# Kernel tuning notes

Hardware: AMD Instinct MI355X
Metric: run time of the kernel (lower is better)

The kernel has to match this reference:

```python
import jax, jax.numpy as jnp
import numpy as np
import math

E = 8          # num_exp
K = 2          # top-k
IN_D = 1024
HD = 2048
BS = 8
SEQ = 2048
CAP_FACTOR = 1.25
MIN_CAP = 4


def setup_inputs() -> dict:
    key = jax.random.key(0)
    ks = jax.random.split(key, 5)
    s = 0.02  # init scale for weights
    x = jax.random.normal(ks[0], (BS, SEQ, IN_D), jnp.float32)
    gate_w = jax.random.normal(ks[1], (E, IN_D), jnp.float32) * s
    fc1_w = jax.random.normal(ks[2], (E, HD, IN_D), jnp.float32) * s
    gating_w = jax.random.normal(ks[3], (E, HD, IN_D), jnp.float32) * s
    fc2_w = jax.random.normal(ks[4], (E, IN_D, HD), jnp.float32) * s
    return {"x": x, "gate_w": gate_w, "fc1_w": fc1_w, "gating_w": gating_w, "fc2_w": fc2_w}


def reference(x, gate_w, fc1_w, gating_w, fc2_w):
    bs, seq, d = x.shape
    N = bs * seq
    NK = N * K
    # capacity in slots per expert (static given shapes)
    capacity = max(int(math.ceil(((NK + E - 1) // E) * CAP_FACTOR)), MIN_CAP)
    dummy = E * capacity  # overflow slot index

    # --- routing ---
    logits = jnp.einsum('bsd,ed->bse', x, gate_w)
    probs = jax.nn.softmax(logits.astype(jnp.float32), axis=-1)
    # load-balancing probs use detached x
    logits_lbl = jnp.einsum('bsd,ed->bse', jax.lax.stop_gradient(x), gate_w)
    probs_lbl = jax.nn.softmax(logits_lbl.astype(jnp.float32), axis=-1)

    topk_vals, topk_inds = jax.lax.top_k(probs, K)          # [bs,seq,K]
    cl = topk_vals / (topk_vals.sum(-1, keepdims=True) + 1e-9)

    x_exp = jnp.repeat(x.reshape(N, d), K, axis=0)          # [NK, d]
    exp_ids = topk_inds.reshape(NK)
    w_flat = cl.reshape(NK).astype(x.dtype)

    # --- dispatch: stable sort by expert id ---
    sort_perm = jnp.argsort(exp_ids * NK + jnp.arange(NK))
    sorted_exp = exp_ids[sort_perm]
    sorted_x = x_exp[sort_perm]
    sorted_w = w_flat[sort_perm]

    counts = jnp.zeros((E,), jnp.int32).at[sorted_exp].add(1)
    starts = jnp.cumsum(counts) - counts
    local_pos = jnp.arange(NK) - starts[sorted_exp]
    keep = local_pos < capacity
    slot = jnp.where(keep, sorted_exp * capacity + local_pos, dummy)

    buf = jnp.zeros((dummy + 1, d), x.dtype).at[slot].set(sorted_x)
    buf_x = buf[:-1].reshape(E, capacity, d)

    # --- per-expert SwiGLU FFN as grouped matmuls ---
    h = jax.nn.silu(jnp.einsum('ecd,ehd->ech', buf_x, fc1_w)) * \
        jnp.einsum('ecd,ehd->ech', buf_x, gating_w)
    buf_out = jnp.einsum('ech,edh->ecd', h, fc2_w)           # [E,cap,d]

    # --- combine ---
    buf_full = jnp.concatenate([buf_out.reshape(dummy, d),
                                jnp.zeros((1, d), x.dtype)], axis=0)
    w_masked = sorted_w * keep.astype(sorted_w.dtype)
    out_sorted = buf_full[slot] * w_masked[:, None]
    out_dispatch = jnp.zeros((NK, d), x.dtype).at[sort_perm].set(out_sorted)
    moe_out = out_dispatch.reshape(N, K, d).sum(axis=1).reshape(bs, seq, d)

    # --- balancing loss ---
    p = probs_lbl.mean(axis=(0, 1))
    f = jax.lax.stop_gradient(
        jnp.zeros((E,), jnp.float32).at[exp_ids].add(1.0) / NK)
    balancing_loss = E * jnp.sum(p * f)
    return moe_out.astype(x.dtype), balancing_loss
```

## Files before the change

kernel.cpp:

```cpp
#include <hip/hip_runtime.h>

#define E_NUM 8
#define DIM   1024
#define HDIM  2048
#define N_TOK 16384
#define NKA   32768
#define CAP   5120
#define REG_SZ 16777216

typedef __bf16 bf16x8 __attribute__((ext_vector_type(8)));
typedef float  f32x4  __attribute__((ext_vector_type(4)));

__device__ __forceinline__ unsigned short f2b(float f) {
  union { float f; unsigned u; } v; v.f = f;
  unsigned r = (v.u + 0x7FFFu + ((v.u >> 16) & 1u)) >> 16;
  return (unsigned short)r;
}

__device__ __forceinline__ void gload16(const void* g, void* l) {
  __builtin_amdgcn_global_load_lds(
      (const __attribute__((address_space(1))) unsigned int*)g,
      (__attribute__((address_space(3))) unsigned int*)l, 16, 0, 0);
}

__global__ __launch_bounds__(256) void cast_kernel(
    const float* __restrict__ s0, const float* __restrict__ s1,
    const float* __restrict__ s2, const float* __restrict__ s3,
    unsigned short* __restrict__ dst) {
  int region = blockIdx.y;
  const float* src = region == 0 ? s0 : region == 1 ? s1 : region == 2 ? s2 : s3;
  size_t i = ((size_t)blockIdx.x * 256 + threadIdx.x) * 8;
  float4 v0 = *(const float4*)(src + i);
  float4 v1 = *(const float4*)(src + i + 4);
  ushort4 u0 = { f2b(v0.x), f2b(v0.y), f2b(v0.z), f2b(v0.w) };
  ushort4 u1 = { f2b(v1.x), f2b(v1.y), f2b(v1.z), f2b(v1.w) };
  unsigned short* o = dst + (size_t)region * REG_SZ + i;
  *(ushort4*)o = u0;
  *(ushort4*)(o + 4) = u1;
}

__global__ __launch_bounds__(256) void routing_kernel(
    const float* __restrict__ x, const float* __restrict__ gate_w,
    int* __restrict__ cnt, float* __restrict__ p_sum,
    int* __restrict__ tok_of_slot, float* __restrict__ w_of_slot) {
  __shared__ float p_acc[E_NUM];
  __shared__ int   lcnt[E_NUM];
  __shared__ int   l_tok[E_NUM][128];
  __shared__ float l_w[E_NUM][128];
  __shared__ int   base[E_NUM];

  int t = threadIdx.x, lane = t & 63, wave = t >> 6;
  if (t < E_NUM) { p_acc[t] = 0.f; lcnt[t] = 0; }
  __syncthreads();

  for (int it = 0; it < 16; ++it) {
    int token = blockIdx.x * 64 + it * 4 + wave;
    const float4* xr = (const float4*)(x + (size_t)token * DIM);
    float4 xv[4];
    #pragma unroll
    for (int i = 0; i < 4; ++i) xv[i] = xr[lane + 64 * i];
    float s[E_NUM];
    #pragma unroll
    for (int e = 0; e < E_NUM; ++e) {
      const float4* gr = (const float4*)(gate_w + e * DIM);
      float acc = 0.f;
      #pragma unroll
      for (int i = 0; i < 4; ++i) {
        float4 g = gr[lane + 64 * i];
        acc += xv[i].x * g.x + xv[i].y * g.y + xv[i].z * g.z + xv[i].w * g.w;
      }
      s[e] = acc;
    }
    #pragma unroll
    for (int e = 0; e < E_NUM; ++e) {
      float v = s[e];
      #pragma unroll
      for (int off = 32; off; off >>= 1) v += __shfl_down(v, off);
      s[e] = v;
    }
    if (lane == 0) {
      float m = s[0];
      #pragma unroll
      for (int e = 1; e < E_NUM; ++e) m = fmaxf(m, s[e]);
      float p[E_NUM]; float sum = 0.f;
      #pragma unroll
      for (int e = 0; e < E_NUM; ++e) { p[e] = expf(s[e] - m); sum += p[e]; }
      float inv = 1.f / sum;
      #pragma unroll
      for (int e = 0; e < E_NUM; ++e) p[e] *= inv;
      int e0 = 0; float v0 = p[0];
      #pragma unroll
      for (int e = 1; e < E_NUM; ++e) if (p[e] > v0) { v0 = p[e]; e0 = e; }
      int e1 = -1; float v1 = -1.f;
      #pragma unroll
      for (int e = 0; e < E_NUM; ++e) if (e != e0 && p[e] > v1) { v1 = p[e]; e1 = e; }
      float denom = v0 + v1 + 1e-9f;
      float w0 = v0 / denom, w1 = v1 / denom;
      #pragma unroll
      for (int e = 0; e < E_NUM; ++e) atomicAdd(&p_acc[e], p[e]);
      int i0 = atomicAdd(&lcnt[e0], 1); l_tok[e0][i0] = token; l_w[e0][i0] = w0;
      int i1 = atomicAdd(&lcnt[e1], 1); l_tok[e1][i1] = token; l_w[e1][i1] = w1;
    }
  }
  __syncthreads();
  if (t < E_NUM) {
    base[t] = atomicAdd(&cnt[t], lcnt[t]);
    atomicAdd(&p_sum[t], p_acc[t]);
  }
  __syncthreads();
  int e = t >> 5, i0 = t & 31;
  int n = lcnt[e], b = base[e];
  for (int i = i0; i < n; i += 32) {
    int pos = b + i;
    if (pos < CAP) {
      tok_of_slot[e * CAP + pos] = l_tok[e][i];
      w_of_slot[e * CAP + pos]   = l_w[e][i];
    }
  }
}

__global__ void loss_kernel(const int* __restrict__ cnt,
                            const float* __restrict__ p_sum,
                            float* __restrict__ out_loss) {
  if (threadIdx.x == 0) {
    float acc = 0.f;
    for (int e = 0; e < E_NUM; ++e)
      acc += (p_sum[e] / (float)N_TOK) * ((float)cnt[e] / (float)NKA);
    *out_loss = (float)E_NUM * acc;
  }
}

__global__ __launch_bounds__(256, 2) void gemm1_kernel(
    const unsigned short* __restrict__ Wb,
    const int* __restrict__ cnt, const int* __restrict__ tok_of_slot,
    unsigned short* __restrict__ Hbuf, int e_base) {
  int ez = blockIdx.z;
  int e = e_base + ez;
  int cntc = min(cnt[e], CAP);
  int m0 = blockIdx.y * 128;
  if (m0 >= cntc) return;
  int n0 = blockIdx.x * 128;

  __shared__ __align__(16) unsigned short As[128 * 32];
  __shared__ __align__(16) unsigned short B1s[128 * 32];
  __shared__ __align__(16) unsigned short B2s[128 * 32];

  int t = threadIdx.x;
  int lane = t & 63, wave = t >> 6;
  int wm = (wave >> 1) * 64, wn = (wave & 1) * 64;
  int quad = lane >> 4, r = lane & 15;

  const unsigned short* W1e = Wb + (size_t)e * HDIM * DIM;
  const unsigned short* Wge = Wb + REG_SZ + (size_t)e * HDIM * DIM;
  const unsigned short* Xb  = Wb + (size_t)3 * REG_SZ;

  int tokA[2];
  #pragma unroll
  for (int i = 0; i < 2; ++i) {
    int row = i * 64 + (t >> 2);
    int slot = m0 + row;
    tokA[i] = (slot < cntc) ? tok_of_slot[e * CAP + slot] : 0;
  }

  f32x4 acc1[4][4], acc2[4][4];
  #pragma unroll
  for (int mt = 0; mt < 4; ++mt)
    #pragma unroll
    for (int nt = 0; nt < 4; ++nt) { acc1[mt][nt] = (f32x4)0.f; acc2[mt][nt] = (f32x4)0.f; }

  for (int k0 = 0; k0 < DIM; k0 += 32) {
    #pragma unroll
    for (int i = 0; i < 2; ++i) {
      int c = i * 256 + t;
      int row = c >> 2, col = (c & 3) * 8;
      int ldsb = (i * 256 + wave * 64) * 8;
      gload16(Xb  + (size_t)tokA[i] * DIM + k0 + col,    &As[ldsb]);
      gload16(W1e + (size_t)(n0 + row) * DIM + k0 + col, &B1s[ldsb]);
      gload16(Wge + (size_t)(n0 + row) * DIM + k0 + col, &B2s[ldsb]);
    }
    __syncthreads();

    bf16x8 af[4], b1f[4], b2f[4];
    #pragma unroll
    for (int mt = 0; mt < 4; ++mt)
      af[mt] = *(const bf16x8*)&As[(wm + mt * 16 + r) * 32 + quad * 8];
    #pragma unroll
    for (int nt = 0; nt < 4; ++nt) {
      b1f[nt] = *(const bf16x8*)&B1s[(wn + nt * 16 + r) * 32 + quad * 8];
      b2f[nt] = *(const bf16x8*)&B2s[(wn + nt * 16 + r) * 32 + quad * 8];
    }
    #pragma unroll
    for (int mt = 0; mt < 4; ++mt)
      #pragma unroll
      for (int nt = 0; nt < 4; ++nt) {
        acc1[mt][nt] = __builtin_amdgcn_mfma_f32_16x16x32_bf16(af[mt], b1f[nt], acc1[mt][nt], 0, 0, 0);
        acc2[mt][nt] = __builtin_amdgcn_mfma_f32_16x16x32_bf16(af[mt], b2f[nt], acc2[mt][nt], 0, 0, 0);
      }
    __syncthreads();
  }

  #pragma unroll
  for (int mt = 0; mt < 4; ++mt) {
    #pragma unroll
    for (int reg = 0; reg < 4; ++reg) {
      int row = m0 + wm + mt * 16 + quad * 4 + reg;
      if (row >= cntc) continue;
      size_t basei = (size_t)(ez * CAP + row) * HDIM + n0;
      #pragma unroll
      for (int nt = 0; nt < 4; ++nt) {
        float a = acc1[mt][nt][reg];
        float b = acc2[mt][nt][reg];
        float h = (a / (1.f + __expf(-a))) * b;
        Hbuf[basei + wn + nt * 16 + r] = f2b(h);
      }
    }
  }
}

__global__ __launch_bounds__(256, 2) void gemm2_kernel(
    const unsigned short* __restrict__ Hbuf, const unsigned short* __restrict__ Wb,
    const int* __restrict__ cnt, const int* __restrict__ tok_of_slot,
    const float* __restrict__ w_of_slot, float* __restrict__ out, int e_base) {
  int ez = blockIdx.z;
  int e = e_base + ez;
  int cntc = min(cnt[e], CAP);
  int m0 = blockIdx.y * 128;
  if (m0 >= cntc) return;
  int n0 = blockIdx.x * 128;

  __shared__ __align__(16) unsigned short As[128 * 32];
  __shared__ __align__(16) unsigned short Bs[128 * 32];

  int t = threadIdx.x;
  int lane = t & 63, wave = t >> 6;
  int wm = (wave >> 1) * 64, wn = (wave & 1) * 64;
  int quad = lane >> 4, r = lane & 15;

  const unsigned short* W2e = Wb + (size_t)2 * REG_SZ + (size_t)e * DIM * HDIM;
  const unsigned short* He  = Hbuf + (size_t)(ez * CAP + m0) * HDIM;

  f32x4 acc[4][4];
  #pragma unroll
  for (int mt = 0; mt < 4; ++mt)
    #pragma unroll
    for (int nt = 0; nt < 4; ++nt) acc[mt][nt] = (f32x4)0.f;

  for (int k0 = 0; k0 < HDIM; k0 += 32) {
    #pragma unroll
    for (int i = 0; i < 2; ++i) {
      int c = i * 256 + t;
      int row = c >> 2, col = (c & 3) * 8;
      int ldsb = (i * 256 + wave * 64) * 8;
      gload16(He  + (size_t)row * HDIM + k0 + col,        &As[ldsb]);
      gload16(W2e + (size_t)(n0 + row) * HDIM + k0 + col, &Bs[ldsb]);
    }
    __syncthreads();

    bf16x8 af[4], bf[4];
    #pragma unroll
    for (int mt = 0; mt < 4; ++mt)
      af[mt] = *(const bf16x8*)&As[(wm + mt * 16 + r) * 32 + quad * 8];
    #pragma unroll
    for (int nt = 0; nt < 4; ++nt)
      bf[nt] = *(const bf16x8*)&Bs[(wn + nt * 16 + r) * 32 + quad * 8];
    #pragma unroll
    for (int mt = 0; mt < 4; ++mt)
      #pragma unroll
      for (int nt = 0; nt < 4; ++nt)
        acc[mt][nt] = __builtin_amdgcn_mfma_f32_16x16x32_bf16(af[mt], bf[nt], acc[mt][nt], 0, 0, 0);
    __syncthreads();
  }

  #pragma unroll
  for (int mt = 0; mt < 4; ++mt) {
    #pragma unroll
    for (int reg = 0; reg < 4; ++reg) {
      int row = m0 + wm + mt * 16 + quad * 4 + reg;
      if (row >= cntc) continue;
      int tok = tok_of_slot[e * CAP + row];
      float w = w_of_slot[e * CAP + row];
      float* orow = out + (size_t)tok * DIM + n0;
      #pragma unroll
      for (int nt = 0; nt < 4; ++nt)
        atomicAdd(&orow[wn + nt * 16 + r], acc[mt][nt][reg] * w);
    }
  }
}

extern "C" void kernel_launch(void* const* d_in, const int* in_sizes, int n_in,
                              void* d_out, int out_size, void* d_ws, size_t ws_size,
                              hipStream_t stream) {
  const float* x        = (const float*)d_in[0];
  const float* gate_w   = (const float*)d_in[1];
  const float* fc1_w    = (const float*)d_in[2];
  const float* gating_w = (const float*)d_in[3];
  const float* fc2_w    = (const float*)d_in[4];
  float* out = (float*)d_out;

  char* ws = (char*)d_ws;
  int*   cnt         = (int*)ws;
  float* p_sum       = (float*)(ws + 128);
  int*   tok_of_slot = (int*)(ws + 256);
  float* w_of_slot   = (float*)(ws + 256 + 163840);
  unsigned short* Wb   = (unsigned short*)(ws + 256 + 2 * 163840);
  size_t hbuf_off = 256 + 2 * 163840 + (size_t)4 * REG_SZ * 2;
  unsigned short* Hbuf = (unsigned short*)(ws + hbuf_off);

  const size_t per_e = (size_t)CAP * HDIM * 2;
  int chunkE = 1;
  if (ws_size > hbuf_off + per_e) {
    size_t c = (ws_size - hbuf_off) / per_e;
    chunkE = c >= 8 ? 8 : (int)c;
  }

  hipMemsetAsync(ws, 0, 256, stream);
  hipMemsetAsync(d_out, 0, (size_t)out_size * sizeof(float), stream);

  cast_kernel<<<dim3(8192, 4), 256, 0, stream>>>(fc1_w, gating_w, fc2_w, x, Wb);
  routing_kernel<<<256, 256, 0, stream>>>(x, gate_w, cnt, p_sum, tok_of_slot, w_of_slot);
  loss_kernel<<<1, 64, 0, stream>>>(cnt, p_sum, out + (size_t)N_TOK * DIM);

  for (int eb = 0; eb < E_NUM; eb += chunkE) {
    int ne = (E_NUM - eb) < chunkE ? (E_NUM - eb) : chunkE;
    gemm1_kernel<<<dim3(16, 40, ne), 256, 0, stream>>>(Wb, cnt, tok_of_slot, Hbuf, eb);
    gemm2_kernel<<<dim3(8, 40, ne), 256, 0, stream>>>(Hbuf, Wb, cnt, tok_of_slot, w_of_slot, out, eb);
  }
}
```

Before: 996.8 us.

## Rewrite expert GEMMs as 256x256 tiles with double-buffered pipelined LDS loads

Both grouped GEMM kernels move from 128x128 tiles with K-step 32 and a sync per step to 256x256 tiles with K-step 64, 512 threads, and a double-buffered LDS pipeline. Quarter-tile loads are interleaved with MFMA phases using explicit vmcnt waits, barriers and setprio. LDS layout is XOR-swizzled to avoid bank conflicts. gemm1 interleaves fc1 and gating rows so each block computes both, and pairs them via lane shuffles in the SwiGLU epilogue. The aims are higher arithmetic intensity and hiding global-load latency, at the cost of large LDS use (128KB), high register pressure, and more tile waste on partially filled expert slots.

Result: faster. 943.5 us (-5.3%).

```diff
diff --git a/kernel.cpp b/kernel.cpp
--- a/kernel.cpp
+++ b/kernel.cpp
@@ -21,6 +21,14 @@
   __builtin_amdgcn_global_load_lds(
       (const __attribute__((address_space(1))) unsigned int*)g,
       (__attribute__((address_space(3))) unsigned int*)l, 16, 0, 0);
+}
+
+template<int N> __device__ __forceinline__ void wait_vmcnt() {
+  if constexpr (N == 10)      asm volatile("s_waitcnt vmcnt(10)" ::: "memory");
+  else if constexpr (N == 8)  asm volatile("s_waitcnt vmcnt(8)"  ::: "memory");
+  else if constexpr (N == 4)  asm volatile("s_waitcnt vmcnt(4)"  ::: "memory");
+  else if constexpr (N == 2)  asm volatile("s_waitcnt vmcnt(2)"  ::: "memory");
+  else if constexpr (N == 0)  asm volatile("s_waitcnt vmcnt(0)"  ::: "memory");
 }
 
 __global__ __launch_bounds__(256) void cast_kernel(
@@ -130,161 +138,225 @@
   }
 }
 
-__global__ __launch_bounds__(256, 2) void gemm1_kernel(
+
+__device__ __forceinline__ void lda_f(const unsigned short* Ab, bf16x8 af[2][4],
+                                      int rowbase, const int cs[2]) {
+  const unsigned short* base = Ab + rowbase * 64;
+  #pragma unroll
+  for (int mt = 0; mt < 4; ++mt) {
+    af[0][mt] = *(const bf16x8*)&base[mt * 1024 + cs[0]];
+    af[1][mt] = *(const bf16x8*)&base[mt * 1024 + cs[1]];
+  }
+}
+__device__ __forceinline__ void ldb_f(const unsigned short* Bb, bf16x8 bf[2][2],
+                                      int rowbase, const int cs[2]) {
+  const unsigned short* base = Bb + rowbase * 64;
+  #pragma unroll
+  for (int nt = 0; nt < 2; ++nt) {
+    bf[0][nt] = *(const bf16x8*)&base[nt * 1024 + cs[0]];
+    bf[1][nt] = *(const bf16x8*)&base[nt * 1024 + cs[1]];
+  }
+}
+
+template<int MH, int NH>
+__device__ __forceinline__ void mmq(f32x4 acc[8][4], const bf16x8 af[2][4],
+                                    const bf16x8 bf[2][2]) {
+  #pragma unroll
+  for (int mt = 0; mt < 4; ++mt)
+    #pragma unroll
+    for (int nt = 0; nt < 2; ++nt) {
+      f32x4 c = acc[MH * 4 + mt][NH * 2 + nt];
+      c = __builtin_amdgcn_mfma_f32_16x16x32_bf16(af[0][mt], bf[0][nt], c, 0, 0, 0);
+      c = __builtin_amdgcn_mfma_f32_16x16x32_bf16(af[1][mt], bf[1][nt], c, 0, 0, 0);
+      acc[MH * 4 + mt][NH * 2 + nt] = c;
+    }
+}
+
+#define A_LDS(b) (&LDS[(b) * 16384])
+#define B_LDS(b) (&LDS[32768 + (b) * 16384])
+
+#define STAGE_A(b, h, kk) { \
+  gload16(srcA[h][0] + (kk) * 64, &LDS[(b) * 16384 + (h) * 8192 + wave * 512]); \
+  gload16(srcA[h][1] + (kk) * 64, &LDS[(b) * 16384 + (h) * 8192 + 4096 + wave * 512]); }
+#define STAGE_B(b, h, kk) { \
+  gload16(srcB[h][0] + (kk) * 64, &LDS[32768 + (b) * 16384 + (h) * 8192 + wave * 512]); \
+  gload16(srcB[h][1] + (kk) * 64, &LDS[32768 + (b) * 16384 + (h) * 8192 + 4096 + wave * 512]); }
+
+#define MIDBAR \
+  __builtin_amdgcn_s_barrier(); \
+  asm volatile("s_waitcnt lgkmcnt(0)" ::: "memory"); \
+  __builtin_amdgcn_sched_barrier(0); \
+  __builtin_amdgcn_s_setprio(1);
+
+#define ENDBAR(W) \
+  __builtin_amdgcn_s_setprio(0); \
+  wait_vmcnt<W>(); \
+  __builtin_amdgcn_s_barrier();
+
+#define TILE_BODY(W1T, W2T, W4T, S1, S2) { \
+  const int cur = kt & 1, oth = cur ^ 1; \
+  lda_f(A_LDS(cur), af, g64r, cs); \
+  ldb_f(B_LDS(cur), bfA, q32r, cs); \
+  if (S1) STAGE_A(oth, 1, kt + 1); \
+  MIDBAR; mmq<0, 0>(acc, af, bfA); ENDBAR(W1T); \
+  ldb_f(B_LDS(cur), bfB, 128 + q32r, cs); \
+  if (S2) STAGE_A(cur, 0, kt + 2); \
+  MIDBAR; mmq<0, 1>(acc, af, bfB); ENDBAR(W2T); \
+  lda_f(A_LDS(cur), af, 128 + g64r, cs); \
+  if (S2) STAGE_B(cur, 0, kt + 2); \
+  MIDBAR; mmq<1, 1>(acc, af, bfB); ENDBAR(-1); \
+  if (S2) STAGE_B(cur, 1, kt + 2); \
+  MIDBAR; mmq<1, 0>(acc, af, bfA); ENDBAR(W4T); \
+}
+
+#define GEMM_PROLOGUE { \
+  STAGE_A(0, 0, 0); STAGE_B(0, 0, 0); STAGE_B(0, 1, 0); STAGE_A(0, 1, 0); \
+  STAGE_A(1, 0, 1); STAGE_B(1, 0, 1); STAGE_B(1, 1, 1); \
+  wait_vmcnt<10>(); \
+  __builtin_amdgcn_s_barrier(); }
+
+#define GEMM_MAIN(NTK) \
+  GEMM_PROLOGUE; \
+  for (int kt = 0; kt < (NTK) - 2; ++kt) TILE_BODY(10, 10, 10, true, true); \
+  { int kt = (NTK) - 2; TILE_BODY(10, 8, 4, true, false); } \
+  { int kt = (NTK) - 1; TILE_BODY(2, 0, -1, false, false); }
+
+__global__ __launch_bounds__(512, 2) void gemm1_kernel(
     const unsigned short* __restrict__ Wb,
     const int* __restrict__ cnt, const int* __restrict__ tok_of_slot,
     unsigned short* __restrict__ Hbuf, int e_base) {
-  int ez = blockIdx.z;
-  int e = e_base + ez;
+  int ez = blockIdx.z, e = e_base + ez;
   int cntc = min(cnt[e], CAP);
-  int m0 = blockIdx.y * 128;
+  int m0 = blockIdx.y * 256;
   if (m0 >= cntc) return;
-  int n0 = blockIdx.x * 128;
-
-  __shared__ __align__(16) unsigned short As[128 * 32];
-  __shared__ __align__(16) unsigned short B1s[128 * 32];
-  __shared__ __align__(16) unsigned short B2s[128 * 32];
-
-  int t = threadIdx.x;
-  int lane = t & 63, wave = t >> 6;
-  int wm = (wave >> 1) * 64, wn = (wave & 1) * 64;
+  int n0 = blockIdx.x * 256;
+
+  __shared__ __align__(16) unsigned short LDS[65536];
+
+  int tid = threadIdx.x;
+  int wave = tid >> 6, lane = tid & 63;
   int quad = lane >> 4, r = lane & 15;
+  int gm = (wave >> 2) * 64, qn = (wave & 3) * 32;
+  int g64r = gm + r, q32r = qn + r;
+  int cs[2] = { (quad ^ (r & 7)) * 8, ((4 + quad) ^ (r & 7)) * 8 };
 
   const unsigned short* W1e = Wb + (size_t)e * HDIM * DIM;
   const unsigned short* Wge = Wb + REG_SZ + (size_t)e * HDIM * DIM;
   const unsigned short* Xb  = Wb + (size_t)3 * REG_SZ;
 
-  int tokA[2];
-  #pragma unroll
-  for (int i = 0; i < 2; ++i) {
-    int row = i * 64 + (t >> 2);
-    int slot = m0 + row;
-    tokA[i] = (slot < cntc) ? tok_of_slot[e * CAP + slot] : 0;
-  }
-
-  f32x4 acc1[4][4], acc2[4][4];
-  #pragma unroll
-  for (int mt = 0; mt < 4; ++mt)
-    #pragma unroll
-    for (int nt = 0; nt < 4; ++nt) { acc1[mt][nt] = (f32x4)0.f; acc2[mt][nt] = (f32x4)0.f; }
-
-  for (int k0 = 0; k0 < DIM; k0 += 32) {
-    #pragma unroll
-    for (int i = 0; i < 2; ++i) {
-      int c = i * 256 + t;
-      int row = c >> 2, col = (c & 3) * 8;
-      int ldsb = (i * 256 + wave * 64) * 8;
-      gload16(Xb  + (size_t)tokA[i] * DIM + k0 + col,    &As[ldsb]);
-      gload16(W1e + (size_t)(n0 + row) * DIM + k0 + col, &B1s[ldsb]);
-      gload16(Wge + (size_t)(n0 + row) * DIM + k0 + col, &B2s[ldsb]);
-    }
-    __syncthreads();
-
-    bf16x8 af[4], b1f[4], b2f[4];
+  const unsigned short* srcA[2][2];
+  const unsigned short* srcB[2][2];
+  #pragma unroll
+  for (int j = 0; j < 2; ++j) {
+    int row = (j * 512 + tid) >> 3;
+    int co  = ((tid & 7) ^ (row & 7)) * 8;
+    #pragma unroll
+    for (int h = 0; h < 2; ++h) {
+      int slot = m0 + h * 128 + row;
+      int tok = (slot < cntc) ? tok_of_slot[e * CAP + slot] : 0;
+      srcA[h][j] = Xb + (size_t)tok * DIM + co;
+      int nglob = n0 + h * 128 + row;
+      const unsigned short* wsrc = (nglob & 1) ? Wge : W1e;
+      srcB[h][j] = wsrc + (size_t)(nglob >> 1) * DIM + co;
+    }
+  }
+
+  f32x4 acc[8][4];
+  #pragma unroll
+  for (int i = 0; i < 8; ++i)
+    #pragma unroll
+    for (int jj = 0; jj < 4; ++jj) acc[i][jj] = (f32x4)0.f;
+  bf16x8 af[2][4], bfA[2][2], bfB[2][2];
+
+  GEMM_MAIN(16);
+
+  #pragma unroll
+  for (int mh = 0; mh < 2; ++mh)
     #pragma unroll
     for (int mt = 0; mt < 4; ++mt)
-      af[mt] = *(const bf16x8*)&As[(wm + mt * 16 + r) * 32 + quad * 8];
-    #pragma unroll
-    for (int nt = 0; nt < 4; ++nt) {
-      b1f[nt] = *(const bf16x8*)&B1s[(wn + nt * 16 + r) * 32 + quad * 8];
-      b2f[nt] = *(const bf16x8*)&B2s[(wn + nt * 16 + r) * 32 + quad * 8];
-    }
-    #pragma unroll
-    for (int mt = 0; mt < 4; ++mt)
-      #pragma unroll
-      for (int nt = 0; nt < 4; ++nt) {
-        acc1[mt][nt] = __builtin_amdgcn_mfma_f32_16x16x32_bf16(af[mt], b1f[nt], acc1[mt][nt], 0, 0, 0);
-        acc2[mt][nt] = __builtin_amdgcn_mfma_f32_16x16x32_bf16(af[mt], b2f[nt], acc2[mt][nt], 0, 0, 0);
+      #pragma unroll
+      for (int reg = 0; reg < 4; ++reg) {
+        int row = m0 + mh * 128 + gm + mt * 16 + quad * 4 + reg;
+        bool wr = (row < cntc);
+        size_t basei = (size_t)(ez * CAP + row) * HDIM;
+        #pragma unroll
+        for (int nh = 0; nh < 2; ++nh)
+          #pragma unroll
+          for (int nt = 0; nt < 2; ++nt) {
+            float v = acc[mh * 4 + mt][nh * 2 + nt][reg];
+            float o = __shfl_xor(v, 1);
+            if (wr && !(lane & 1)) {
+              float a = v, b = o;
+              float hval = (a / (1.f + __expf(-a))) * b;
+              int coln = n0 + nh * 128 + qn + nt * 16 + r;
+              Hbuf[basei + (coln >> 1)] = f2b(hval);
+            }
+          }
       }
-    __syncthreads();
-  }
-
-  #pragma unroll
-  for (int mt = 0; mt < 4; ++mt) {
-    #pragma unroll
-    for (int reg = 0; reg < 4; ++reg) {
-      int row = m0 + wm + mt * 16 + quad * 4 + reg;
-      if (row >= cntc) continue;
-      size_t basei = (size_t)(ez * CAP + row) * HDIM + n0;
-      #pragma unroll
-      for (int nt = 0; nt < 4; ++nt) {
-        float a = acc1[mt][nt][reg];
-        float b = acc2[mt][nt][reg];
-        float h = (a / (1.f + __expf(-a))) * b;
-        Hbuf[basei + wn + nt * 16 + r] = f2b(h);
-      }
-    }
-  }
-}
-
-__global__ __launch_bounds__(256, 2) void gemm2_kernel(
+}
+
+__global__ __launch_bounds__(512, 2) void gemm2_kernel(
     const unsigned short* __restrict__ Hbuf, const unsigned short* __restrict__ Wb,
     const int* __restrict__ cnt, const int* __restrict__ tok_of_slot,
     const float* __restrict__ w_of_slot, float* __restrict__ out, int e_base) {
-  int ez = blockIdx.z;
-  int e = e_base + ez;
+  int ez = blockIdx.z, e = e_base + ez;
   int cntc = min(cnt[e], CAP);
-  int m0 = blockIdx.y * 128;
+  int m0 = blockIdx.y * 256;
   if (m0 >= cntc) return;
-  int n0 = blockIdx.x * 128;
-
-  __shared__ __align__(16) unsigned short As[128 * 32];
-  __shared__ __align__(16) unsigned short Bs[128 * 32];
-
-  int t = threadIdx.x;
-  int lane = t & 63, wave = t >> 6;
-  int wm = (wave >> 1) * 64, wn = (wave & 1) * 64;
+  int n0 = blockIdx.x * 256;
+
+  __shared__ __align__(16) unsigned short LDS[65536];
+
+  int tid = threadIdx.x;
+  int wave = tid >> 6, lane = tid & 63;
   int quad = lane >> 4, r = lane & 15;
+  int gm = (wave >> 2) * 64, qn = (wave & 3) * 32;
+  int g64r = gm + r, q32r = qn + r;
+  int cs[2] = { (quad ^ (r & 7)) * 8, ((4 + quad) ^ (r & 7)) * 8 };
 
   const unsigned short* W2e = Wb + (size_t)2 * REG_SZ + (size_t)e * DIM * HDIM;
-  const unsigned short* He  = Hbuf + (size_t)(ez * CAP + m0) * HDIM;
-
-  f32x4 acc[4][4];
-  #pragma unroll
-  for (int mt = 0; mt < 4; ++mt)
-    #pragma unroll
-    for (int nt = 0; nt < 4; ++nt) acc[mt][nt] = (f32x4)0.f;
-
-  for (int k0 = 0; k0 < HDIM; k0 += 32) {
-    #pragma unroll
-    for (int i = 0; i < 2; ++i) {
-      int c = i * 256 + t;
-      int row = c >> 2, col = (c & 3) * 8;
-      int ldsb = (i * 256 + wave * 64) * 8;
-      gload16(He  + (size_t)row * HDIM + k0 + col,        &As[ldsb]);
-      gload16(W2e + (size_t)(n0 + row) * HDIM + k0 + col, &Bs[ldsb]);
-    }
-    __syncthreads();
-
-    bf16x8 af[4], bf[4];
+  const unsigned short* He  = Hbuf + (size_t)(ez * CAP) * HDIM;
+
+  const unsigned short* srcA[2][2];
+  const unsigned short* srcB[2][2];
+  #pragma unroll
+  for (int j = 0; j < 2; ++j) {
+    int row = (j * 512 + tid) >> 3;
+    int co  = ((tid & 7) ^ (row & 7)) * 8;
+    #pragma unroll
+    for (int h = 0; h < 2; ++h) {
+      srcA[h][j] = He + (size_t)(m0 + h * 128 + row) * HDIM + co;
+      srcB[h][j] = W2e + (size_t)(n0 + h * 128 + row) * HDIM + co;
+    }
+  }
+
+  f32x4 acc[8][4];
+  #pragma unroll
+  for (int i = 0; i < 8; ++i)
+    #pragma unroll
+    for (int jj = 0; jj < 4; ++jj) acc[i][jj] = (f32x4)0.f;
+  bf16x8 af[2][4], bfA[2][2], bfB[2][2];
+
+  GEMM_MAIN(32);
+
+  #pragma unroll
+  for (int mh = 0; mh < 2; ++mh)
     #pragma unroll
     for (int mt = 0; mt < 4; ++mt)
-      af[mt] = *(const bf16x8*)&As[(wm + mt * 16 + r) * 32 + quad * 8];
-    #pragma unroll
-    for (int nt = 0; nt < 4; ++nt)
-      bf[nt] = *(const bf16x8*)&Bs[(wn + nt * 16 + r) * 32 + quad * 8];
-    #pragma unroll
-    for (int mt = 0; mt < 4; ++mt)
-      #pragma unroll
-      for (int nt = 0; nt < 4; ++nt)
-        acc[mt][nt] = __builtin_amdgcn_mfma_f32_16x16x32_bf16(af[mt], bf[nt], acc[mt][nt], 0, 0, 0);
-    __syncthreads();
-  }
-
-  #pragma unroll
-  for (int mt = 0; mt < 4; ++mt) {
-    #pragma unroll
-    for (int reg = 0; reg < 4; ++reg) {
-      int row = m0 + wm + mt * 16 + quad * 4 + reg;
-      if (row >= cntc) continue;
-      int tok = tok_of_slot[e * CAP + row];
-      float w = w_of_slot[e * CAP + row];
-      float* orow = out + (size_t)tok * DIM + n0;
-      #pragma unroll
-      for (int nt = 0; nt < 4; ++nt)
-        atomicAdd(&orow[wn + nt * 16 + r], acc[mt][nt][reg] * w);
-    }
-  }
+      #pragma unroll
+      for (int reg = 0; reg < 4; ++reg) {
+        int rowl = m0 + mh * 128 + gm + mt * 16 + quad * 4 + reg;
+        if (rowl >= cntc) continue;
+        int tok = tok_of_slot[e * CAP + rowl];
+        float w = w_of_slot[e * CAP + rowl];
+        float* orow = out + (size_t)tok * DIM + n0;
+        #pragma unroll
+        for (int nh = 0; nh < 2; ++nh)
+          #pragma unroll
+          for (int nt = 0; nt < 2; ++nt)
+            atomicAdd(&orow[nh * 128 + qn + nt * 16 + r],
+                      acc[mh * 4 + mt][nh * 2 + nt][reg] * w);
+      }
 }
 
 extern "C" void kernel_launch(void* const* d_in, const int* in_sizes, int n_in,
@@ -322,7 +394,7 @@
 
   for (int eb = 0; eb < E_NUM; eb += chunkE) {
     int ne = (E_NUM - eb) < chunkE ? (E_NUM - eb) : chunkE;
-    gemm1_kernel<<<dim3(16, 40, ne), 256, 0, stream>>>(Wb, cnt, tok_of_slot, Hbuf, eb);
-    gemm2_kernel<<<dim3(8, 40, ne), 256, 0, stream>>>(Hbuf, Wb, cnt, tok_of_slot, w_of_slot, out, eb);
-  }
-}
+    gemm1_kernel<<<dim3(16, 20, ne), 512, 0, stream>>>(Wb, cnt, tok_of_slot, Hbuf, eb);
+    gemm2_kernel<<<dim3(4, 20, ne), 512, 0, stream>>>(Hbuf, Wb, cnt, tok_of_slot, w_of_slot, out, eb);
+  }
+}
```
